# Optimization experiments

Measured on AMD Instinct MI355X. Metric: run time of the kernel, lower is better.

Reference implementation:

```python
import jax, jax.numpy as jnp
import numpy as np

N = 500_000
E = 8_000_000
IN, HID, OUT = 1, 10, 4
BN_EPS = 1e-5


def _lin_init(key, fan_in, fan_out):
    kw, kb = jax.random.split(key)
    s = 1.0 / np.sqrt(fan_in)
    W = jax.random.uniform(kw, (fan_in, fan_out), minval=-s, maxval=s, dtype=jnp.float32)
    b = jax.random.uniform(kb, (fan_out,), minval=-s, maxval=s, dtype=jnp.float32)
    return W, b


def setup_inputs() -> dict:
    key = jax.random.key(0)
    ks = jax.random.split(key, 12)
    x = jax.random.normal(ks[0], (N, IN), dtype=jnp.float32)
    edge_index = jax.random.randint(ks[1], (2, E), 0, N, dtype=jnp.int64)
    edge_attr = jax.random.uniform(ks[2], (E,), dtype=jnp.float32)
    inp = {"x": x, "edge_index": edge_index, "edge_attr": edge_attr}
    dims = [(IN, HID), (HID, HID), (HID, HID)]
    for i, (di, do) in enumerate(dims, start=1):
        k1, k2 = jax.random.split(ks[2 + i])
        W1, b1 = _lin_init(k1, di, do)
        W2, b2 = _lin_init(k2, do, do)
        inp[f"W{i}a"], inp[f"b{i}a"] = W1, b1
        inp[f"W{i}b"], inp[f"b{i}b"] = W2, b2
        inp[f"g{i}"] = jnp.ones((do,), jnp.float32)
        inp[f"be{i}"] = jnp.zeros((do,), jnp.float32)
    Wf, bf = _lin_init(ks[10], 3 * HID, OUT)
    inp["Wf"], inp["bf"] = Wf, bf
    return inp


def _gin_layer(x, src, dst, Wa, ba, Wb, bb, g, be):
    # GINConv (eps=0): h_i = MLP(x_i + sum_{j->i} x_j); Linear->Linear->BatchNorm (train mode)
    agg = jax.ops.segment_sum(x[src], dst, num_segments=N)  # [N, d]
    h = x + agg
    h = h @ Wa + ba
    h = h @ Wb + bb
    mu = jnp.mean(h, axis=0)
    var = jnp.var(h, axis=0)
    return g * (h - mu) * jax.lax.rsqrt(var + BN_EPS) + be


def _modularity(s, src, dst, w):
    two_m = jnp.sum(w)
    pos = jnp.sum(w * jnp.sum(s[src] * s[dst], axis=-1)) / two_m
    deg = jax.ops.segment_sum(w, src, num_segments=N)  # [N]
    ds = (deg @ s) / two_m  # [OUT]
    return pos - jnp.sum(ds * ds)


def reference(x, edge_index, edge_attr,
              W1a, b1a, W1b, b1b, g1, be1,
              W2a, b2a, W2b, b2b, g2, be2,
              W3a, b3a, W3b, b3b, g3, be3,
              Wf, bf):
    src, dst = edge_index[0], edge_index[1]
    x11 = _gin_layer(x, src, dst, W1a, b1a, W1b, b1b, g1, be1)
    x12 = _gin_layer(x11, src, dst, W2a, b2a, W2b, b2b, g2, be2)
    x13 = _gin_layer(x12, src, dst, W3a, b3a, W3b, b3b, g3, be3)
    logits = jnp.concatenate([x11, x12, x13], axis=-1) @ Wf + bf
    s = jax.nn.softmax(logits, axis=-1)
    q = _modularity(s, src, dst, edge_attr)
    return s, q
```

## Files before the change

### kernel.cpp

```cpp
#include <hip/hip_runtime.h>
#include <hip/hip_bf16.h>

#define NN 500000
#define NE 8000000
#define NB 123
#define BSH 12
#define BSZ 4096
#define CAP 69632
#define M 8
#define NAGG (NB * M)
#define BN_EPS 1e-5f

typedef unsigned uv4 __attribute__((ext_vector_type(4)));
typedef float fv4 __attribute__((ext_vector_type(4)));
typedef unsigned long long u64;

__device__ __forceinline__ float waveReduceF(float v) {
#pragma unroll
    for (int o = 32; o > 0; o >>= 1) v += __shfl_down(v, o, 64);
    return v;
}
__device__ __forceinline__ double waveReduceD(double v) {
#pragma unroll
    for (int o = 32; o > 0; o >>= 1) v += __shfl_down(v, o, 64);
    return v;
}
__device__ __forceinline__ float u2f(unsigned short u) {
    return __bfloat162float(__builtin_bit_cast(__hip_bfloat16, u));
}
__device__ __forceinline__ unsigned short f2u(float f) {
    return __builtin_bit_cast(unsigned short, __float2bfloat16(f));
}
__device__ __forceinline__ u64 pk1(float v) {
    int iv = (int)rintf(v * 268435456.f);
    return ((u64)(long long)iv << 20) + 1ull;
}

__global__ void initk(int* __restrict__ cur)
{
    if (threadIdx.x < NB) cur[threadIdx.x] = (int)threadIdx.x * CAP;
}

__global__ __launch_bounds__(512) void scatterk(
    const int4* __restrict__ src4, const int4* __restrict__ dst4,
    const float4* __restrict__ w4, int* __restrict__ cur,
    unsigned* __restrict__ pairs, unsigned short* __restrict__ wp)
{
    __shared__ unsigned sEnt[4096];
    __shared__ unsigned short sW[4096];
    __shared__ unsigned char sB[4096];
    __shared__ int h[8][128];
    __shared__ int wOff[8][128];
    __shared__ int bOff[128];
    __shared__ int lb[128];
    __shared__ int tot[128];

    int tid = threadIdx.x, wv = tid >> 6;
    for (int j = tid; j < 8 * 128; j += 512) (&h[0][0])[j] = 0;
    __syncthreads();

    unsigned en[8]; unsigned short wb[8]; int rb[8];
#pragma unroll
    for (int k = 0; k < 2; k++) {
        int q = blockIdx.x * 1024 + k * 512 + tid;
        if (q < NE / 4) {
            int4 s4 = src4[q]; int4 d4 = dst4[q]; float4 ww = w4[q];
            int ss[4] = {s4.x, s4.y, s4.z, s4.w};
            int dd[4] = {d4.x, d4.y, d4.z, d4.w};
            float fw[4] = {ww.x, ww.y, ww.z, ww.w};
#pragma unroll
            for (int i = 0; i < 4; i++) {
                int d = dd[i], b = d >> BSH;
                en[k * 4 + i] = ((unsigned)(d & (BSZ - 1)) << 19) | (unsigned)ss[i];
                wb[k * 4 + i] = f2u(fw[i]);
                int rk = atomicAdd(&h[wv][b], 1);
                rb[k * 4 + i] = (rk << 8) | b;
            }
        } else {
#pragma unroll
            for (int i = 0; i < 4; i++) rb[k * 4 + i] = -1;
        }
    }
    __syncthreads();
    if (tid < NB) {
        int acc = 0;
#pragma unroll
        for (int w = 0; w < 8; w++) { wOff[w][tid] = acc; acc += h[w][tid]; }
        tot[tid] = acc;
        lb[tid] = atomicAdd(&cur[tid], acc);
    }
    __syncthreads();
    if (tid == 0) {
        int acc = 0;
        for (int b = 0; b < NB; b++) { bOff[b] = acc; acc += tot[b]; }
    }
    __syncthreads();
#pragma unroll
    for (int k = 0; k < 8; k++) {
        if (rb[k] >= 0) {
            int b = rb[k] & 255, rk = rb[k] >> 8;
            int pos = bOff[b] + wOff[wv][b] + rk;
            sEnt[pos] = en[k]; sW[pos] = wb[k]; sB[pos] = (unsigned char)b;
        }
    }
    __syncthreads();
    int nE = NE - blockIdx.x * 4096; if (nE > 4096) nE = 4096;
    for (int j = tid; j < nE; j += 512) {
        int b = sB[j];
        int glob = lb[b] + (j - bOff[b]);
        pairs[glob] = sEnt[j];
        wp[glob] = sW[j];
    }
}

__global__ __launch_bounds__(512) void agg1k(
    const unsigned* __restrict__ pairs, const int* __restrict__ cur,
    const float* __restrict__ x, u64* __restrict__ slab)
{
    __shared__ u64 t[BSZ];
    for (int j = threadIdx.x; j < BSZ; j += 512) t[j] = 0ull;
    __syncthreads();
    int B = blockIdx.x / M, sl = blockIdx.x % M;
    int b0 = B * CAP;
    int len = cur[B] - b0;
    int seg = (((len + M - 1) / M) + 3) & ~3;
    int lo = b0 + sl * seg;
    int hi = lo + seg, e1 = b0 + len;
    if (hi > e1) hi = e1;
    int n = hi - lo;
    if (n > 0) {
        int nq = n >> 2;
        const uv4* pq = (const uv4*)(pairs + lo);
        for (int i = threadIdx.x; i < nq; i += 1024) {
            uv4 pA = __builtin_nontemporal_load(pq + i);
            int iB = i + 512;
            bool vB = iB < nq;
            float a0 = x[pA.x & 524287u];
            float a1 = x[pA.y & 524287u];
            float a2 = x[pA.z & 524287u];
            float a3 = x[pA.w & 524287u];
            float c0, c1, c2, c3; unsigned d4, d5, d6, d7;
            if (vB) {
                uv4 pB = __builtin_nontemporal_load(pq + iB);
                c0 = x[pB.x & 524287u]; d4 = pB.x >> 19;
                c1 = x[pB.y & 524287u]; d5 = pB.y >> 19;
                c2 = x[pB.z & 524287u]; d6 = pB.z >> 19;
                c3 = x[pB.w & 524287u]; d7 = pB.w >> 19;
            }
            atomicAdd(&t[pA.x >> 19], pk1(a0));
            atomicAdd(&t[pA.y >> 19], pk1(a1));
            atomicAdd(&t[pA.z >> 19], pk1(a2));
            atomicAdd(&t[pA.w >> 19], pk1(a3));
            if (vB) {
                atomicAdd(&t[d4], pk1(c0));
                atomicAdd(&t[d5], pk1(c1));
                atomicAdd(&t[d6], pk1(c2));
                atomicAdd(&t[d7], pk1(c3));
            }
        }
        int rem = n & 3;
        if ((int)threadIdx.x < rem) {
            unsigned p = pairs[lo + (nq << 2) + threadIdx.x];
            atomicAdd(&t[p >> 19], pk1(x[p & 524287u]));
        }
    }
    __syncthreads();
    u64* sb = slab + (size_t)blockIdx.x * BSZ;
    for (int j = threadIdx.x; j < BSZ; j += 512)
        __builtin_nontemporal_store(t[j], sb + j);
}

__global__ __launch_bounds__(256) void mergeN1(
    const u64* __restrict__ slab, const float* __restrict__ x,
    float2* __restrict__ UN2, u64* __restrict__ ENC)
{
    int i = blockIdx.x * 256 + threadIdx.x;
    if (i >= NN) return;
    int B = i >> BSH, low = i & (BSZ - 1);
    u64 s = 0ull;
#pragma unroll
    for (int m = 0; m < M; m++)
        s += __builtin_nontemporal_load(slab + (size_t)(B * M + m) * BSZ + low);
    unsigned cn = (unsigned)(s & 0xFFFFFull);
    long long sv = (long long)(s - (u64)cn) >> 20;
    float u = x[i] + (float)((double)sv * 3.725290298461914e-09);
    UN2[i] = make_float2(u, (float)cn);
    long long iu = (long long)rintf(u * 67108864.f);
    ENC[i] = ((u64)iu << 22) + (u64)cn;
}

__global__ __launch_bounds__(512) void agg2k(
    const unsigned* __restrict__ pairs, const int* __restrict__ cur,
    const u64* __restrict__ ENC, u64* __restrict__ slab)
{
    __shared__ u64 t[BSZ];
    for (int j = threadIdx.x; j < BSZ; j += 512) t[j] = 0ull;
    __syncthreads();
    int B = blockIdx.x / M, sl = blockIdx.x % M;
    int b0 = B * CAP;
    int len = cur[B] - b0;
    int seg = (((len + M - 1) / M) + 3) & ~3;
    int lo = b0 + sl * seg;
    int hi = lo + seg, e1 = b0 + len;
    if (hi > e1) hi = e1;
    int n = hi - lo;
    if (n > 0) {
        int nq = n >> 2;
        const uv4* pq = (const uv4*)(pairs + lo);
        for (int i = threadIdx.x; i < nq; i += 1024) {
            uv4 pA = __builtin_nontemporal_load(pq + i);
            int iB = i + 512;
            bool vB = iB < nq;
            u64 e0 = ENC[pA.x & 524287u];
            u64 e1v = ENC[pA.y & 524287u];
            u64 e2 = ENC[pA.z & 524287u];
            u64 e3 = ENC[pA.w & 524287u];
            u64 e4, e5, e6, e7; unsigned d4, d5, d6, d7;
            if (vB) {
                uv4 pB = __builtin_nontemporal_load(pq + iB);
                e4 = ENC[pB.x & 524287u]; d4 = pB.x >> 19;
                e5 = ENC[pB.y & 524287u]; d5 = pB.y >> 19;
                e6 = ENC[pB.z & 524287u]; d6 = pB.z >> 19;
                e7 = ENC[pB.w & 524287u]; d7 = pB.w >> 19;
            }
            atomicAdd(&t[pA.x >> 19], e0);
            atomicAdd(&t[pA.y >> 19], e1v);
            atomicAdd(&t[pA.z >> 19], e2);
            atomicAdd(&t[pA.w >> 19], e3);
            if (vB) {
                atomicAdd(&t[d4], e4);
                atomicAdd(&t[d5], e5);
                atomicAdd(&t[d6], e6);
                atomicAdd(&t[d7], e7);
            }
        }
        int rem = n & 3;
        if ((int)threadIdx.x < rem) {
            unsigned p = pairs[lo + (nq << 2) + threadIdx.x];
            atomicAdd(&t[p >> 19], ENC[p & 524287u]);
        }
    }
    __syncthreads();
    u64* sb = slab + (size_t)blockIdx.x * BSZ;
    for (int j = threadIdx.x; j < BSZ; j += 512)
        __builtin_nontemporal_store(t[j], sb + j);
}

__global__ __launch_bounds__(256) void mergeN2(
    const u64* __restrict__ slab, float* __restrict__ SU, float* __restrict__ SN)
{
    int i = blockIdx.x * 256 + threadIdx.x;
    if (i >= NN) return;
    int B = i >> BSH, low = i & (BSZ - 1);
    u64 s = 0ull;
#pragma unroll
    for (int m = 0; m < M; m++)
        s += __builtin_nontemporal_load(slab + (size_t)(B * M + m) * BSZ + low);
    unsigned sn = (unsigned)(s & 0x3FFFFFull);
    long long sv = (long long)(s - (u64)sn) >> 22;
    float su = (float)((double)sv * 1.4901161193847656e-08);
    SU[i] = su;
    SN[i] = (float)sn;
}

__global__ __launch_bounds__(512) void agg3k(
    const unsigned* __restrict__ pairs, const int* __restrict__ cur,
    const float* __restrict__ SU, float* __restrict__ slab)
{
    __shared__ float t[BSZ];
    for (int j = threadIdx.x; j < BSZ; j += 512) t[j] = 0.f;
    __syncthreads();
    int B = blockIdx.x / M, sl = blockIdx.x % M;
    int b0 = B * CAP;
    int len = cur[B] - b0;
    int seg = (((len + M - 1) / M) + 3) & ~3;
    int lo = b0 + sl * seg;
    int hi = lo + seg, e1 = b0 + len;
    if (hi > e1) hi = e1;
    int n = hi - lo;
    if (n > 0) {
        int nq = n >> 2;
        const uv4* pq = (const uv4*)(pairs + lo);
        for (int i = threadIdx.x; i < nq; i += 1024) {
            uv4 pA = __builtin_nontemporal_load(pq + i);
            int iB = i + 512;
            bool vB = iB < nq;
            float a0 = SU[pA.x & 524287u];
            float a1 = SU[pA.y & 524287u];
            float a2 = SU[pA.z & 524287u];
            float a3 = SU[pA.w & 524287u];
            float c0, c1, c2, c3; unsigned d4, d5, d6, d7;
            if (vB) {
                uv4 pB = __builtin_nontemporal_load(pq + iB);
                c0 = SU[pB.x & 524287u]; d4 = pB.x >> 19;
                c1 = SU[pB.y & 524287u]; d5 = pB.y >> 19;
                c2 = SU[pB.z & 524287u]; d6 = pB.z >> 19;
                c3 = SU[pB.w & 524287u]; d7 = pB.w >> 19;
            }
            atomicAdd(&t[pA.x >> 19], a0);
            atomicAdd(&t[pA.y >> 19], a1);
            atomicAdd(&t[pA.z >> 19], a2);
            atomicAdd(&t[pA.w >> 19], a3);
            if (vB) {
                atomicAdd(&t[d4], c0);
                atomicAdd(&t[d5], c1);
                atomicAdd(&t[d6], c2);
                atomicAdd(&t[d7], c3);
            }
        }
        int rem = n & 3;
        if ((int)threadIdx.x < rem) {
            unsigned p = pairs[lo + (nq << 2) + threadIdx.x];
            atomicAdd(&t[p >> 19], SU[p & 524287u]);
        }
    }
    __syncthreads();
    float* sb = slab + (size_t)blockIdx.x * BSZ;
    for (int j = threadIdx.x; j < BSZ; j += 512)
        __builtin_nontemporal_store(t[j], sb + j);
}

__global__ __launch_bounds__(256) void m3mom(
    const float* __restrict__ slab, const float2* __restrict__ UN2,
    const float* __restrict__ SU, const float* __restrict__ SN,
    float* __restrict__ SSU, double* __restrict__ dm)
{
    int i = blockIdx.x * 256 + threadIdx.x;
    double z[5] = {0, 0, 0, 0, 0};
    if (i < NN) {
        int B = i >> BSH, low = i & (BSZ - 1);
        float ssu = 0.f;
#pragma unroll
        for (int m = 0; m < M; m++)
            ssu += __builtin_nontemporal_load(slab + (size_t)(B * M + m) * BSZ + low);
        SSU[i] = ssu;
        float2 un = UN2[i];
        z[0] = (double)un.x; z[1] = (double)un.y; z[2] = (double)SU[i];
        z[3] = (double)SN[i]; z[4] = (double)ssu;
    }
    double m[20];
#pragma unroll
    for (int a = 0; a < 5; a++) m[a] = z[a];
    int idx = 5;
#pragma unroll
    for (int a = 0; a < 5; a++)
#pragma unroll
        for (int b = a; b < 5; b++) m[idx++] = z[a] * z[b];

    __shared__ double part[4][20];
    int lane = threadIdx.x & 63, wid = threadIdx.x >> 6;
#pragma unroll
    for (int k = 0; k < 20; k++) {
        double r = waveReduceD(m[k]);
        if (lane == 0) part[wid][k] = r;
    }
    __syncthreads();
    if (threadIdx.x < 20)
        atomicAdd(&dm[threadIdx.x],
                  part[0][threadIdx.x] + part[1][threadIdx.x] +
                  part[2][threadIdx.x] + part[3][threadIdx.x]);
}

__device__ void mm1010(const float* in, const float* Wa, const float* Wb, float* out)
{
    float t[10];
    for (int m = 0; m < 10; m++) {
        float acc = 0.f;
        for (int k = 0; k < 10; k++) acc += in[k] * Wa[k * 10 + m];
        t[m] = acc;
    }
    for (int j = 0; j < 10; j++) {
        float acc = 0.f;
        for (int m = 0; m < 10; m++) acc += t[m] * Wb[m * 10 + j];
        out[j] = acc;
    }
}

__global__ void constk(
    const float* __restrict__ W1a, const float* __restrict__ b1a,
    const float* __restrict__ W1b, const float* __restrict__ b1b,
    const float* __restrict__ g1, const float* __restrict__ be1,
    const float* __restrict__ W2a, const float* __restrict__ b2a,
    const float* __restrict__ W2b, const float* __restrict__ b2b,
    const float* __restrict__ g2, const float* __restrict__ be2,
    const float* __restrict__ W3a, const float* __restrict__ b3a,
    const float* __restrict__ W3b, const float* __restrict__ b3b,
    const float* __restrict__ g3, const float* __restrict__ be3,
    const float* __restrict__ Wf, const float* __restrict__ bf_,
    const double* __restrict__ dm, float* __restrict__ Lout)
{
    if (threadIdx.x != 0 || blockIdx.x != 0) return;
    const double invN = 1.0 / (double)NN;
    double E[5];
    for (int m = 0; m < 5; m++) E[m] = dm[m] * invN;
    double C[5][5];
    {
        int idx = 5;
        for (int a = 0; a < 5; a++)
            for (int b = a; b < 5; b++) {
                double c = dm[idx++] * invN - E[a] * E[b];
                C[a][b] = c; C[b][a] = c;
            }
    }
    float v[10], c1[10];
    for (int j = 0; j < 10; j++) {
        float av = 0.f, ac = 0.f;
        for (int k = 0; k < 10; k++) {
            av += W1a[k] * W1b[k * 10 + j];
            ac += b1a[k] * W1b[k * 10 + j];
        }
        v[j] = av; c1[j] = ac + b1b[j];
    }
    double Eu = E[0], Vu = C[0][0];
    float p[10], q[10];
    for (int j = 0; j < 10; j++) {
        float var1 = (float)(Vu * (double)v[j] * (double)v[j]);
        float sc1 = g1[j] * rsqrtf(var1 + BN_EPS);
        p[j] = sc1 * v[j];
        q[j] = be1[j] - (float)Eu * p[j];
    }
    float r[10], s[10], d2[10];
    mm1010(p, W2a, W2b, r);
    mm1010(q, W2a, W2b, s);
    for (int j = 0; j < 10; j++) {
        float acc = b2b[j];
        for (int m = 0; m < 10; m++) acc += b2a[m] * W2b[m * 10 + j];
        d2[j] = acc;
    }
    double Ea = E[0] + E[2], Eb = 1.0 + E[1];
    double Va = C[0][0] + 2.0 * C[0][2] + C[2][2];
    double Vb = C[1][1];
    double Cab = C[0][1] + C[2][1];
    float rt[10], st[10], dt[10];
    for (int j = 0; j < 10; j++) {
        double rj = r[j], sj = s[j];
        float var2 = (float)(Va * rj * rj + Vb * sj * sj + 2.0 * Cab * rj * sj);
        float sc2 = g2[j] * rsqrtf(var2 + BN_EPS);
        rt[j] = sc2 * r[j];
        st[j] = sc2 * s[j];
        dt[j] = be2[j] - sc2 * (float)(Ea * rj + Eb * sj);
    }
    float r3[10], s3[10], t3[10], d3[10];
    mm1010(rt, W3a, W3b, r3);
    mm1010(st, W3a, W3b, s3);
    mm1010(dt, W3a, W3b, t3);
    for (int j = 0; j < 10; j++) {
        float acc = b3b[j];
        for (int m = 0; m < 10; m++) acc += b3a[m] * W3b[m * 10 + j];
        d3[j] = acc;
    }
    const double gA[5] = {1, 0, 2, 0, 1};
    const double gB[5] = {0, 2, 0, 1, 0};
    const double gC[5] = {0, 1, 0, 0, 0};
    double EA = E[0] + 2.0 * E[2] + E[4];
    double EB = 1.0 + 2.0 * E[1] + E[3];
    double EC = 1.0 + E[1];
    double VA = 0, VB = 0, VC = 0, CAB = 0, CAC = 0, CBC = 0;
    for (int a = 0; a < 5; a++)
        for (int b = 0; b < 5; b++) {
            double c = C[a][b];
            VA  += gA[a] * gA[b] * c;
            VB  += gB[a] * gB[b] * c;
            VC  += gC[a] * gC[b] * c;
            CAB += gA[a] * gB[b] * c;
            CAC += gA[a] * gC[b] * c;
            CBC += gB[a] * gC[b] * c;
        }
    float rh[10], sh[10], th[10], dh[10];
    for (int j = 0; j < 10; j++) {
        double rj = r3[j], sj = s3[j], tj = t3[j];
        float var3 = (float)(VA * rj * rj + VB * sj * sj + VC * tj * tj
                             + 2.0 * (CAB * rj * sj + CAC * rj * tj + CBC * sj * tj));
        float sc3 = g3[j] * rsqrtf(var3 + BN_EPS);
        rh[j] = sc3 * r3[j];
        sh[j] = sc3 * s3[j];
        th[j] = sc3 * t3[j];
        dh[j] = be3[j] - sc3 * (float)(EA * rj + EB * sj + EC * tj);
    }
    for (int k = 0; k < 4; k++) {
        float Lu = 0, Ln = 0, Lsu = 0, Lsn = 0, Lssu = 0, L0 = bf_[k];
        for (int j = 0; j < 10; j++) {
            float wf1 = Wf[j * 4 + k];
            float wf2 = Wf[(10 + j) * 4 + k];
            float wf3 = Wf[(20 + j) * 4 + k];
            Lu   += p[j] * wf1 + rt[j] * wf2 + rh[j] * wf3;
            Ln   += st[j] * wf2 + (2.f * sh[j] + th[j]) * wf3;
            Lsu  += rt[j] * wf2 + 2.f * rh[j] * wf3;
            Lsn  += sh[j] * wf3;
            Lssu += rh[j] * wf3;
            L0   += q[j] * wf1 + (st[j] + dt[j]) * wf2 + (sh[j] + th[j] + dh[j]) * wf3;
        }
        Lout[0 * 4 + k] = Lu;  Lout[1 * 4 + k] = Ln;   Lout[2 * 4 + k] = Lsu;
        Lout[3 * 4 + k] = Lsn; Lout[4 * 4 + k] = Lssu; Lout[5 * 4 + k] = L0;
    }
}

__global__ __launch_bounds__(256) void finalk(
    const float2* __restrict__ UN2, const float* __restrict__ SU,
    const float* __restrict__ SN, const float* __restrict__ SSU,
    const float* __restrict__ L,
    float4* __restrict__ sout, ushort4* __restrict__ sbf)
{
    __shared__ float sL[24];
    if (threadIdx.x < 24) sL[threadIdx.x] = L[threadIdx.x];
    __syncthreads();
    int i = blockIdx.x * 256 + threadIdx.x;
    if (i >= NN) return;
    float2 un = UN2[i];
    float u = un.x, n = un.y, su = SU[i], sn = SN[i], ssu = SSU[i];
    float lg[4];
#pragma unroll
    for (int k = 0; k < 4; k++)
        lg[k] = sL[k] * u + sL[4 + k] * n + sL[8 + k] * su
              + sL[12 + k] * sn + sL[16 + k] * ssu + sL[20 + k];
    float mx = fmaxf(fmaxf(lg[0], lg[1]), fmaxf(lg[2], lg[3]));
    float e0 = __expf(lg[0] - mx), e1 = __expf(lg[1] - mx);
    float e2 = __expf(lg[2] - mx), e3 = __expf(lg[3] - mx);
    float inv = 1.f / (e0 + e1 + e2 + e3);
    float s0 = e0 * inv, s1 = e1 * inv, s2 = e2 * inv, s3 = e3 * inv;
    fv4 o = {s0, s1, s2, s3};
    __builtin_nontemporal_store(o, (fv4*)sout + i);
    ushort4 pk; pk.x = f2u(s0); pk.y = f2u(s1); pk.z = f2u(s2); pk.w = f2u(s3);
    sbf[i] = pk;
}

__device__ __forceinline__ void modacc(u64 ua, u64 ub, float we, float* acc) {
    float ax = u2f((unsigned short)ua),         ay = u2f((unsigned short)(ua >> 16));
    float az = u2f((unsigned short)(ua >> 32)), aw = u2f((unsigned short)(ua >> 48));
    float bx = u2f((unsigned short)ub),         by = u2f((unsigned short)(ub >> 16));
    float bz = u2f((unsigned short)(ub >> 32)), bw = u2f((unsigned short)(ub >> 48));
    acc[0] += we;
    acc[1] += we * (ax * bx + ay * by + az * bz + aw * bw);
    acc[2] += we * ax; acc[3] += we * ay;
    acc[4] += we * az; acc[5] += we * aw;
}

__global__ __launch_bounds__(512) void modk(
    const unsigned* __restrict__ pairs, const unsigned short* __restrict__ wp,
    const int* __restrict__ cur, const u64* __restrict__ sbfU,
    float* __restrict__ scal)
{
    __shared__ u64 sS[BSZ];
    int B = blockIdx.x / M, sl = blockIdx.x % M;
    for (int j = threadIdx.x; j < BSZ; j += 512) {
        int g = (B << BSH) + j;
        sS[j] = (g < NN) ? sbfU[g] : 0ull;
    }
    __syncthreads();
    int b0 = B * CAP;
    int len = cur[B] - b0;
    int seg = (((len + M - 1) / M) + 3) & ~3;
    int lo = b0 + sl * seg;
    int hi = lo + seg, e1 = b0 + len;
    if (hi > e1) hi = e1;
    int n = hi - lo;
    float acc[6] = {0, 0, 0, 0, 0, 0};
    if (n > 0) {
        int nq = n >> 2;
        const uv4* pq = (const uv4*)(pairs + lo);
        const u64* wq = (const u64*)(wp + lo);
        for (int i = threadIdx.x; i < nq; i += 1024) {
            uv4 pA = __builtin_nontemporal_load(pq + i);
            u64 wA = __builtin_nontemporal_load(wq + i);
            int iB = i + 512;
            bool vB = iB < nq;
            u64 a0 = sbfU[pA.x & 524287u];
            u64 a1 = sbfU[pA.y & 524287u];
            u64 a2 = sbfU[pA.z & 524287u];
            u64 a3 = sbfU[pA.w & 524287u];
            uv4 pB; u64 wB; u64 a4, a5, a6, a7;
            if (vB) {
                pB = __builtin_nontemporal_load(pq + iB);
                wB = __builtin_nontemporal_load(wq + iB);
                a4 = sbfU[pB.x & 524287u];
                a5 = sbfU[pB.y & 524287u];
                a6 = sbfU[pB.z & 524287u];
                a7 = sbfU[pB.w & 524287u];
            }
            modacc(a0, sS[pA.x >> 19], u2f((unsigned short)wA),         acc);
            modacc(a1, sS[pA.y >> 19], u2f((unsigned short)(wA >> 16)), acc);
            modacc(a2, sS[pA.z >> 19], u2f((unsigned short)(wA >> 32)), acc);
            modacc(a3, sS[pA.w >> 19], u2f((unsigned short)(wA >> 48)), acc);
            if (vB) {
                modacc(a4, sS[pB.x >> 19], u2f((unsigned short)wB),         acc);
                modacc(a5, sS[pB.y >> 19], u2f((unsigned short)(wB >> 16)), acc);
                modacc(a6, sS[pB.z >> 19], u2f((unsigned short)(wB >> 32)), acc);
                modacc(a7, sS[pB.w >> 19], u2f((unsigned short)(wB >> 48)), acc);
            }
        }
        int rem = n & 3;
        if ((int)threadIdx.x < rem) {
            int idx = lo + (nq << 2) + threadIdx.x;
            unsigned p = pairs[idx];
            modacc(sbfU[p & 524287u], sS[p >> 19], u2f(wp[idx]), acc);
        }
    }
    __shared__ float part[8][6];
    int lane = threadIdx.x & 63, wid = threadIdx.x >> 6;
#pragma unroll
    for (int k = 0; k < 6; k++) {
        float r = waveReduceF(acc[k]);
        if (lane == 0) part[wid][k] = r;
    }
    __syncthreads();
    if (threadIdx.x < 6) {
        float vsum = 0.f;
#pragma unroll
        for (int wdi = 0; wdi < 8; wdi++) vsum += part[wdi][threadIdx.x];
        int off = (threadIdx.x == 0) ? 128 : (threadIdx.x == 1 ? 129 : 130 + threadIdx.x);
        atomicAdd(&scal[off], vsum);
    }
}

__global__ void qk(const float* __restrict__ scal, float* __restrict__ out)
{
    if (threadIdx.x == 0) {
        float inv = 1.f / scal[128];
        float posv = scal[129] * inv;
        float acc = 0.f;
#pragma unroll
        for (int k = 0; k < 4; k++) {
            float d = scal[132 + k] * inv;
            acc += d * d;
        }
        out[(size_t)NN * 4] = posv - acc;
    }
}

extern "C" void kernel_launch(void* const* d_in, const int* in_sizes, int n_in,
                              void* d_out, int out_size, void* d_ws, size_t ws_size,
                              hipStream_t stream) {
    const float* x  = (const float*)d_in[0];
    const int*  ei  = (const int*)d_in[1];
    const int*  src = ei;
    const int*  dst = ei + NE;
    const float* w   = (const float*)d_in[2];
    const float* W1a = (const float*)d_in[3];  const float* b1a = (const float*)d_in[4];
    const float* W1b = (const float*)d_in[5];  const float* b1b = (const float*)d_in[6];
    const float* g1  = (const float*)d_in[7];  const float* be1 = (const float*)d_in[8];
    const float* W2a = (const float*)d_in[9];  const float* b2a = (const float*)d_in[10];
    const float* W2b = (const float*)d_in[11]; const float* b2b = (const float*)d_in[12];
    const float* g2  = (const float*)d_in[13]; const float* be2 = (const float*)d_in[14];
    const float* W3a = (const float*)d_in[15]; const float* b3a = (const float*)d_in[16];
    const float* W3b = (const float*)d_in[17]; const float* b3b = (const float*)d_in[18];
    const float* g3  = (const float*)d_in[19]; const float* be3 = (const float*)d_in[20];
    const float* Wf  = (const float*)d_in[21]; const float* bfb = (const float*)d_in[22];

    float*  sc   = (float*)d_ws;
    int*    sci  = (int*)d_ws;
    double* dm   = (double*)(sc + 384);
    unsigned* pairs = (unsigned*)(sc + 1024);
    unsigned short* wp = (unsigned short*)(pairs + (size_t)NB * CAP);
    float*  slab = (float*)(wp + (size_t)NB * CAP);
    u64*    slabU = (u64*)slab;
    float2* UN2  = (float2*)(slab + (size_t)NAGG * 2 * BSZ);
    float*  SU   = (float*)(UN2 + NN);
    float*  SN   = SU + NN;
    float*  SSU  = SN + NN;
    ushort4* sbf = (ushort4*)(SSU + NN);
    u64*    ENC  = (u64*)(sbf + NN);
    float*  sout = (float*)d_out;

    const int NB_N  = (NN + 255) / 256;
    const int NB_EQ = (NE / 4 + 1023) / 1024;

    hipMemsetAsync(sc, 0, 4096, stream);
    initk<<<1, 128, 0, stream>>>(sci + 832);

    scatterk<<<NB_EQ, 512, 0, stream>>>((const int4*)src, (const int4*)dst,
                                        (const float4*)w, sci + 832, pairs, wp);

    agg1k<<<NAGG, 512, 0, stream>>>(pairs, sci + 832, x, slabU);
    mergeN1<<<NB_N, 256, 0, stream>>>(slabU, x, UN2, ENC);
    agg2k<<<NAGG, 512, 0, stream>>>(pairs, sci + 832, ENC, slabU);
    mergeN2<<<NB_N, 256, 0, stream>>>(slabU, SU, SN);
    agg3k<<<NAGG, 512, 0, stream>>>(pairs, sci + 832, SU, slab);
    m3mom<<<NB_N, 256, 0, stream>>>(slab, UN2, SU, SN, SSU, dm);

    constk<<<1, 64, 0, stream>>>(W1a, b1a, W1b, b1b, g1, be1,
                                 W2a, b2a, W2b, b2b, g2, be2,
                                 W3a, b3a, W3b, b3b, g3, be3,
                                 Wf, bfb, dm, sc + 160);
    finalk<<<NB_N, 256, 0, stream>>>(UN2, SU, SN, SSU, sc + 160, (float4*)sout, sbf);
    modk<<<NAGG, 512, 0, stream>>>(pairs, wp, sci + 832, (const u64*)sbf, sc);
    qk<<<1, 64, 0, stream>>>(sc, sout);
}
```

Measured before the change: 496.6 us.

## Fuse merge passes into aggregation kernels via last-block reduction and drop init/q kernels

Removes the separate mergeN1/mergeN2 kernels: each bucket's last-finishing slice block (tracked with an atomic counter and threadfence) merges the partial slabs and writes UN2/ENC or SU/SN. The final modularity scalar is likewise computed by the last modk block, removing the qk launch. The initk launch goes away because bucket cursors now start at zero from the memset and get offset by tid*CAP. Scatter also gets nontemporal loads/stores and a wave-scan for bucket offsets. Together this cuts kernel launches and serial gaps, at the cost of tail work on single blocks and extra atomics/fences.

```diff
diff --git a/kernel.cpp b/kernel.cpp
--- a/kernel.cpp
+++ b/kernel.cpp
@@ -12,6 +12,7 @@
 #define BN_EPS 1e-5f
 
 typedef unsigned uv4 __attribute__((ext_vector_type(4)));
+typedef int iv4 __attribute__((ext_vector_type(4)));
 typedef float fv4 __attribute__((ext_vector_type(4)));
 typedef unsigned long long u64;
 
@@ -36,14 +37,9 @@
     return ((u64)(long long)iv << 20) + 1ull;
 }
 
-__global__ void initk(int* __restrict__ cur)
-{
-    if (threadIdx.x < NB) cur[threadIdx.x] = (int)threadIdx.x * CAP;
-}
-
 __global__ __launch_bounds__(512) void scatterk(
-    const int4* __restrict__ src4, const int4* __restrict__ dst4,
-    const float4* __restrict__ w4, int* __restrict__ cur,
+    const iv4* __restrict__ src4, const iv4* __restrict__ dst4,
+    const fv4* __restrict__ w4, int* __restrict__ cur,
     unsigned* __restrict__ pairs, unsigned short* __restrict__ wp)
 {
     __shared__ unsigned sEnt[4096];
@@ -64,7 +60,9 @@
     for (int k = 0; k < 2; k++) {
         int q = blockIdx.x * 1024 + k * 512 + tid;
         if (q < NE / 4) {
-            int4 s4 = src4[q]; int4 d4 = dst4[q]; float4 ww = w4[q];
+            iv4 s4 = __builtin_nontemporal_load(src4 + q);
+            iv4 d4 = __builtin_nontemporal_load(dst4 + q);
+            fv4 ww = __builtin_nontemporal_load(w4 + q);
             int ss[4] = {s4.x, s4.y, s4.z, s4.w};
             int dd[4] = {d4.x, d4.y, d4.z, d4.w};
             float fw[4] = {ww.x, ww.y, ww.z, ww.w};
@@ -87,12 +85,22 @@
 #pragma unroll
         for (int w = 0; w < 8; w++) { wOff[w][tid] = acc; acc += h[w][tid]; }
         tot[tid] = acc;
-        lb[tid] = atomicAdd(&cur[tid], acc);
-    }
-    __syncthreads();
-    if (tid == 0) {
-        int acc = 0;
-        for (int b = 0; b < NB; b++) { bOff[b] = acc; acc += tot[b]; }
+        lb[tid] = tid * CAP + atomicAdd(&cur[tid], acc);
+    }
+    __syncthreads();
+    if (tid < 64) {
+        int lane = tid;
+        int a = (2 * lane < NB) ? tot[2 * lane] : 0;
+        int b = (2 * lane + 1 < NB) ? tot[2 * lane + 1] : 0;
+        int s = a + b;
+#pragma unroll
+        for (int o = 1; o < 64; o <<= 1) {
+            int t = __shfl_up(s, o, 64);
+            if (lane >= o) s += t;
+        }
+        int excl = s - (a + b);
+        bOff[2 * lane] = excl;
+        bOff[2 * lane + 1] = excl + a;
     }
     __syncthreads();
 #pragma unroll
@@ -108,21 +116,23 @@
     for (int j = tid; j < nE; j += 512) {
         int b = sB[j];
         int glob = lb[b] + (j - bOff[b]);
-        pairs[glob] = sEnt[j];
-        wp[glob] = sW[j];
+        __builtin_nontemporal_store(sEnt[j], pairs + glob);
+        __builtin_nontemporal_store(sW[j], wp + glob);
     }
 }
 
 __global__ __launch_bounds__(512) void agg1k(
     const unsigned* __restrict__ pairs, const int* __restrict__ cur,
-    const float* __restrict__ x, u64* __restrict__ slab)
+    const float* __restrict__ x, u64* __restrict__ slab, int* __restrict__ cnt1,
+    float2* __restrict__ UN2, u64* __restrict__ ENC)
 {
     __shared__ u64 t[BSZ];
+    __shared__ int lastS;
     for (int j = threadIdx.x; j < BSZ; j += 512) t[j] = 0ull;
     __syncthreads();
     int B = blockIdx.x / M, sl = blockIdx.x % M;
     int b0 = B * CAP;
-    int len = cur[B] - b0;
+    int len = cur[B];
     int seg = (((len + M - 1) / M) + 3) & ~3;
     int lo = b0 + sl * seg;
     int hi = lo + seg, e1 = b0 + len;
@@ -166,39 +176,44 @@
     }
     __syncthreads();
     u64* sb = slab + (size_t)blockIdx.x * BSZ;
-    for (int j = threadIdx.x; j < BSZ; j += 512)
-        __builtin_nontemporal_store(t[j], sb + j);
-}
-
-__global__ __launch_bounds__(256) void mergeN1(
-    const u64* __restrict__ slab, const float* __restrict__ x,
-    float2* __restrict__ UN2, u64* __restrict__ ENC)
-{
-    int i = blockIdx.x * 256 + threadIdx.x;
-    if (i >= NN) return;
-    int B = i >> BSH, low = i & (BSZ - 1);
-    u64 s = 0ull;
-#pragma unroll
-    for (int m = 0; m < M; m++)
-        s += __builtin_nontemporal_load(slab + (size_t)(B * M + m) * BSZ + low);
-    unsigned cn = (unsigned)(s & 0xFFFFFull);
-    long long sv = (long long)(s - (u64)cn) >> 20;
-    float u = x[i] + (float)((double)sv * 3.725290298461914e-09);
-    UN2[i] = make_float2(u, (float)cn);
-    long long iu = (long long)rintf(u * 67108864.f);
-    ENC[i] = ((u64)iu << 22) + (u64)cn;
+    for (int j = threadIdx.x; j < BSZ; j += 512) sb[j] = t[j];
+    __threadfence();
+    __syncthreads();
+    if (threadIdx.x == 0)
+        lastS = (atomicAdd(&cnt1[B], 1) == M - 1) ? 1 : 0;
+    __syncthreads();
+    if (lastS) {
+        int base = B << BSH;
+        for (int j = threadIdx.x; j < BSZ; j += 512) {
+            int node = base + j;
+            if (node >= NN) continue;
+            u64 s = 0ull;
+#pragma unroll
+            for (int m = 0; m < M; m++)
+                s += __hip_atomic_load(&slab[(size_t)(B * M + m) * BSZ + j],
+                                       __ATOMIC_RELAXED, __HIP_MEMORY_SCOPE_AGENT);
+            unsigned cn = (unsigned)(s & 0xFFFFFull);
+            long long sv = (long long)(s - (u64)cn) >> 20;
+            float u = x[node] + (float)((double)sv * 3.725290298461914e-09);
+            UN2[node] = make_float2(u, (float)cn);
+            long long iu = (long long)rintf(u * 67108864.f);
+            ENC[node] = ((u64)iu << 22) + (u64)cn;
+        }
+    }
 }
 
 __global__ __launch_bounds__(512) void agg2k(
     const unsigned* __restrict__ pairs, const int* __restrict__ cur,
-    const u64* __restrict__ ENC, u64* __restrict__ slab)
+    const u64* __restrict__ ENC, u64* __restrict__ slab, int* __restrict__ cnt2,
+    float* __restrict__ SU, float* __restrict__ SN)
 {
     __shared__ u64 t[BSZ];
+    __shared__ int lastS;
     for (int j = threadIdx.x; j < BSZ; j += 512) t[j] = 0ull;
     __syncthreads();
     int B = blockIdx.x / M, sl = blockIdx.x % M;
     int b0 = B * CAP;
-    int len = cur[B] - b0;
+    int len = cur[B];
     int seg = (((len + M - 1) / M) + 3) & ~3;
     int lo = b0 + sl * seg;
     int hi = lo + seg, e1 = b0 + len;
@@ -242,25 +257,29 @@
     }
     __syncthreads();
     u64* sb = slab + (size_t)blockIdx.x * BSZ;
-    for (int j = threadIdx.x; j < BSZ; j += 512)
-        __builtin_nontemporal_store(t[j], sb + j);
-}
-
-__global__ __launch_bounds__(256) void mergeN2(
-    const u64* __restrict__ slab, float* __restrict__ SU, float* __restrict__ SN)
-{
-    int i = blockIdx.x * 256 + threadIdx.x;
-    if (i >= NN) return;
-    int B = i >> BSH, low = i & (BSZ - 1);
-    u64 s = 0ull;
-#pragma unroll
-    for (int m = 0; m < M; m++)
-        s += __builtin_nontemporal_load(slab + (size_t)(B * M + m) * BSZ + low);
-    unsigned sn = (unsigned)(s & 0x3FFFFFull);
-    long long sv = (long long)(s - (u64)sn) >> 22;
-    float su = (float)((double)sv * 1.4901161193847656e-08);
-    SU[i] = su;
-    SN[i] = (float)sn;
+    for (int j = threadIdx.x; j < BSZ; j += 512) sb[j] = t[j];
+    __threadfence();
+    __syncthreads();
+    if (threadIdx.x == 0)
+        lastS = (atomicAdd(&cnt2[B], 1) == M - 1) ? 1 : 0;
+    __syncthreads();
+    if (lastS) {
+        int base = B << BSH;
+        for (int j = threadIdx.x; j < BSZ; j += 512) {
+            int node = base + j;
+            if (node >= NN) continue;
+            u64 s = 0ull;
+#pragma unroll
+            for (int m = 0; m < M; m++)
+                s += __hip_atomic_load(&slab[(size_t)(B * M + m) * BSZ + j],
+                                       __ATOMIC_RELAXED, __HIP_MEMORY_SCOPE_AGENT);
+            unsigned sn = (unsigned)(s & 0x3FFFFFull);
+            long long sv = (long long)(s - (u64)sn) >> 22;
+            float su = (float)((double)sv * 1.4901161193847656e-08);
+            SU[node] = su;
+            SN[node] = (float)sn;
+        }
+    }
 }
 
 __global__ __launch_bounds__(512) void agg3k(
@@ -272,7 +291,7 @@
     __syncthreads();
     int B = blockIdx.x / M, sl = blockIdx.x % M;
     int b0 = B * CAP;
-    int len = cur[B] - b0;
+    int len = cur[B];
     int seg = (((len + M - 1) / M) + 3) & ~3;
     int lo = b0 + sl * seg;
     int hi = lo + seg, e1 = b0 + len;
@@ -535,10 +554,10 @@
     acc[4] += we * az; acc[5] += we * aw;
 }
 
-__global__ __launch_bounds__(512) void modk(
+__global__ __launch_bounds__(512) void modkQ(
     const unsigned* __restrict__ pairs, const unsigned short* __restrict__ wp,
     const int* __restrict__ cur, const u64* __restrict__ sbfU,
-    float* __restrict__ scal)
+    float* __restrict__ scal, int* __restrict__ cnt, float* __restrict__ outq)
 {
     __shared__ u64 sS[BSZ];
     int B = blockIdx.x / M, sl = blockIdx.x % M;
@@ -548,7 +567,7 @@
     }
     __syncthreads();
     int b0 = B * CAP;
-    int len = cur[B] - b0;
+    int len = cur[B];
     int seg = (((len + M - 1) / M) + 3) & ~3;
     int lo = b0 + sl * seg;
     int hi = lo + seg, e1 = b0 + len;
@@ -609,21 +628,23 @@
         for (int wdi = 0; wdi < 8; wdi++) vsum += part[wdi][threadIdx.x];
         int off = (threadIdx.x == 0) ? 128 : (threadIdx.x == 1 ? 129 : 130 + threadIdx.x);
         atomicAdd(&scal[off], vsum);
-    }
-}
-
-__global__ void qk(const float* __restrict__ scal, float* __restrict__ out)
-{
+        __threadfence();
+    }
+    __syncthreads();
     if (threadIdx.x == 0) {
-        float inv = 1.f / scal[128];
-        float posv = scal[129] * inv;
-        float acc = 0.f;
-#pragma unroll
-        for (int k = 0; k < 4; k++) {
-            float d = scal[132 + k] * inv;
-            acc += d * d;
-        }
-        out[(size_t)NN * 4] = posv - acc;
+        if (atomicAdd(cnt, 1) == (int)gridDim.x - 1) {
+            float tm = atomicAdd(&scal[128], 0.f);
+            float pos = atomicAdd(&scal[129], 0.f);
+            float inv = 1.f / tm;
+            float posv = pos * inv;
+            float acq = 0.f;
+#pragma unroll
+            for (int k = 0; k < 4; k++) {
+                float d = atomicAdd(&scal[132 + k], 0.f) * inv;
+                acq += d * d;
+            }
+            outq[(size_t)NN * 4] = posv - acq;
+        }
     }
 }
 
@@ -665,15 +686,12 @@
     const int NB_EQ = (NE / 4 + 1023) / 1024;
 
     hipMemsetAsync(sc, 0, 4096, stream);
-    initk<<<1, 128, 0, stream>>>(sci + 832);
-
-    scatterk<<<NB_EQ, 512, 0, stream>>>((const int4*)src, (const int4*)dst,
-                                        (const float4*)w, sci + 832, pairs, wp);
-
-    agg1k<<<NAGG, 512, 0, stream>>>(pairs, sci + 832, x, slabU);
-    mergeN1<<<NB_N, 256, 0, stream>>>(slabU, x, UN2, ENC);
-    agg2k<<<NAGG, 512, 0, stream>>>(pairs, sci + 832, ENC, slabU);
-    mergeN2<<<NB_N, 256, 0, stream>>>(slabU, SU, SN);
+
+    scatterk<<<NB_EQ, 512, 0, stream>>>((const iv4*)src, (const iv4*)dst,
+                                        (const fv4*)w, sci + 832, pairs, wp);
+
+    agg1k<<<NAGG, 512, 0, stream>>>(pairs, sci + 832, x, slabU, sci + 448, UN2, ENC);
+    agg2k<<<NAGG, 512, 0, stream>>>(pairs, sci + 832, ENC, slabU, sci + 576, SU, SN);
     agg3k<<<NAGG, 512, 0, stream>>>(pairs, sci + 832, SU, slab);
     m3mom<<<NB_N, 256, 0, stream>>>(slab, UN2, SU, SN, SSU, dm);
 
@@ -681,7 +699,8 @@
                                  W2a, b2a, W2b, b2b, g2, be2,
                                  W3a, b3a, W3b, b3b, g3, be3,
                                  Wf, bfb, dm, sc + 160);
+
     finalk<<<NB_N, 256, 0, stream>>>(UN2, SU, SN, SSU, sc + 160, (float4*)sout, sbf);
-    modk<<<NAGG, 512, 0, stream>>>(pairs, wp, sci + 832, (const u64*)sbf, sc);
-    qk<<<1, 64, 0, stream>>>(sc, sout);
-}
+    modkQ<<<NAGG, 512, 0, stream>>>(pairs, wp, sci + 832, (const u64*)sbf, sc,
+                                    sci + 961, sout);
+}
```

Result: slower. 1.117 ms (+124.9%).
